# Optimization experiments

Hardware: AMD Instinct MI355X
Metric: run time of the kernel (lower is better)

Reference implementation:

```python
import jax, jax.numpy as jnp
import numpy as np

LAYER_BS = 63
N_SITES = 12
B = 2048


def _kaiming_uniform(key, shape, fan_in):
    # torch kaiming_uniform_ with a=0: bound = sqrt(6/fan_in)
    bound = np.sqrt(6.0 / fan_in)
    return jax.random.uniform(key, shape, jnp.float32, -bound, bound)


def _cnn12(x, w):
    # x: (B, L, 12, Cin); w: (L, 3*Cin, Cout)
    nn0 = jnp.roll(x, -1, axis=-2) + jnp.roll(x, 3, axis=-2)
    nnn0 = jnp.roll(x, -2, axis=-2) + jnp.roll(x, 4, axis=-2)
    c0 = jnp.concatenate([nn0, nnn0], axis=-1)          # (B,L,12,2*Cin)
    c1 = c0 + jnp.roll(c0, -2, axis=-2)
    allc = jnp.concatenate([x, c1], axis=-1)            # (B,L,12,3*Cin)
    return jnp.einsum('blsc,lco->blso', allc, w)


def _batch_linear(x, w, b):
    # x: (B, L, F); w: (L, F, O); b: (L, O)
    return jnp.einsum('blf,lfo->blo', x, w) + b


def setup_inputs() -> dict:
    key = jax.random.key(0)
    ks = jax.random.split(key, 9)
    zs = jax.random.normal(ks[0], (B, LAYER_BS, N_SITES, 2), jnp.float32)
    # CNN weights: (L, 3*Cin, Cout); kaiming fan_in = 3*Cin
    w1 = _kaiming_uniform(ks[1], (LAYER_BS, 6, 32), 6)
    w2 = _kaiming_uniform(ks[2], (LAYER_BS, 96, 64), 96)
    fw1 = _kaiming_uniform(ks[3], (LAYER_BS, 128, 64), 128)
    fb1 = jax.random.uniform(ks[4], (LAYER_BS, 64), jnp.float32, -1 / np.sqrt(128), 1 / np.sqrt(128))
    fw2 = _kaiming_uniform(ks[5], (LAYER_BS, 64, 64), 64)
    fb2 = jax.random.uniform(ks[6], (LAYER_BS, 64), jnp.float32, -1 / np.sqrt(64), 1 / np.sqrt(64))
    fw3 = _kaiming_uniform(ks[7], (LAYER_BS, 64, 1), 64)
    fb3 = jax.random.uniform(ks[8], (LAYER_BS, 1), jnp.float32, -1 / np.sqrt(64), 1 / np.sqrt(64))
    return {"zs": zs, "w1": w1, "w2": w2, "fw1": fw1, "fb1": fb1,
            "fw2": fw2, "fb2": fb2, "fw3": fw3, "fb3": fb3}


def reference(zs, w1, w2, fw1, fb1, fw2, fb2, fw3, fb3):
    h = jax.nn.relu(_cnn12(zs, w1))                     # (B,L,12,32)
    h = jax.nn.relu(_cnn12(h, w2))                      # (B,L,12,64)
    h = jnp.concatenate([h.mean(axis=-2), h.max(axis=-2)], axis=-1)
    h = jax.nn.relu(_batch_linear(h, fw1, fb1))
    h = jax.nn.relu(_batch_linear(h, fw2, fb2))
    out = _batch_linear(h, fw3, fb3)                    # (B,L,1)
    return out[..., 0]                                  # (B,L)
```

## Files before the change

### kernel.cpp

```cpp
#include <hip/hip_runtime.h>


#define LNUM 63
#define BT 16
#define NBT 128
#define WSL 19968

typedef __attribute__((ext_vector_type(8))) _Float16 half8;
typedef __attribute__((ext_vector_type(2))) _Float16 half2v;
typedef __attribute__((ext_vector_type(4))) float floatx4;
typedef __attribute__((ext_vector_type(4))) unsigned uint4v;

static __device__ __forceinline__ unsigned cvtpk(float a, float b) {
    return __builtin_bit_cast(unsigned, __builtin_amdgcn_cvt_pkrtz(a, b));
}
static __device__ __forceinline__ half2v u2h(unsigned u) { return __builtin_bit_cast(half2v, u); }
static __device__ __forceinline__ unsigned h2u(half2v h) { return __builtin_bit_cast(unsigned, h); }
static __device__ __forceinline__ float hlo16(unsigned short s) {
    return (float)__builtin_bit_cast(_Float16, s);
}
static __device__ __forceinline__ int w12(int v) { return v >= 12 ? v - 12 : v; }
static __device__ __forceinline__ float2 add2(float2 a, float2 b) { return make_float2(a.x + b.x, a.y + b.y); }

#define O_POOLDW 3072
#define O_POOLUS 6144
#define O_POOL2  0
#define O_G2     1280

__global__ void prep(const float* __restrict__ w2, const float* __restrict__ fw1,
                     const float* __restrict__ fw2, unsigned short* __restrict__ ws) {
    const int l = blockIdx.x, t = threadIdx.x;
    const int o = t & 63, g = t >> 6;
    if (blockIdx.y == 0) {
        unsigned* w2t = (unsigned*)(ws + (size_t)l * WSL);
        const float* w2l = w2 + (size_t)l * 6144;
        #pragma unroll
        for (int i = 0; i < 12; ++i) {
            int cp = g + 4 * i, c = 2 * cp;
            w2t[o * 52 + cp] = cvtpk(w2l[c * 64 + o], w2l[(c + 1) * 64 + o]);
        }
    } else {
        unsigned* f1t = (unsigned*)(ws + (size_t)l * WSL + 6656);
        const float* f1l = fw1 + (size_t)l * 8192;
        #pragma unroll
        for (int i = 0; i < 16; ++i) {
            int cp = g + 4 * i;
            f1t[o * 68 + cp] = cvtpk(f1l[cp * 64 + o], f1l[(64 + cp) * 64 + o]);
        }
        unsigned* f2t = (unsigned*)(ws + (size_t)l * WSL + 15360);
        const float* f2l = fw2 + (size_t)l * 4096;
        #pragma unroll
        for (int i = 0; i < 8; ++i) {
            int cp = g + 4 * i, c = 2 * cp;
            f2t[o * 36 + cp] = cvtpk(f2l[c * 64 + o], f2l[(c + 1) * 64 + o]);
        }
    }
}

__global__ __launch_bounds__(256, 4) void fused_nn(
    const float* __restrict__ zs,  const float* __restrict__ w1,
    const float* __restrict__ fb1, const float* __restrict__ fb2,
    const float* __restrict__ fw3, const float* __restrict__ fb3,
    const unsigned short* __restrict__ ws,
    float* __restrict__ out)
{
    __shared__ __align__(16) unsigned U[4160];
    unsigned short* USH = (unsigned short*)U;

    const int t    = threadIdx.x;
    const int lane = t & 63;
    const int wv   = t >> 6;
    const int n    = lane & 15;
    const int quad = lane >> 4;
    const int l    = blockIdx.x / NBT;
    const int b0   = (blockIdx.x % NBT) * BT;

    {
        const int b = t >> 4, cpair = t & 15, c0 = cpair * 2;
        const float* xb = zs + ((size_t)(b0 + b) * LNUM + l) * 24;
        float4 xq[6];
        #pragma unroll
        for (int q = 0; q < 6; ++q) xq[q] = *(const float4*)(xb + q * 4);
        float2 xv[12], xr[12], xA[12], xB[12];
        #pragma unroll
        for (int s = 0; s < 12; ++s)
            xv[s] = (s & 1) ? make_float2(xq[s >> 1].z, xq[s >> 1].w)
                            : make_float2(xq[s >> 1].x, xq[s >> 1].y);
        #pragma unroll
        for (int s = 0; s < 12; ++s) xr[s] = add2(xv[w12(s + 1)], xv[w12(s + 11)]);
        #pragma unroll
        for (int s = 0; s < 12; ++s) {
            xA[s] = add2(xr[w12(s + 2)], xr[w12(s + 10)]);
            xB[s] = add2(xr[w12(s + 3)], xr[w12(s + 9)]);
        }
        const float* wl = w1 + (size_t)l * 192 + c0;
        const float2 w0  = *(const float2*)(wl);
        const float2 w1v = *(const float2*)(wl + 32);
        const float2 w2v = *(const float2*)(wl + 64);
        const float2 w3v = *(const float2*)(wl + 96);
        const float2 w4v = *(const float2*)(wl + 128);
        const float2 w5v = *(const float2*)(wl + 160);
        #pragma unroll
        for (int s = 0; s < 12; ++s) {
            float hx = xv[s].x*w0.x + xv[s].y*w1v.x + xA[s].x*w2v.x + xA[s].y*w3v.x
                     + xB[s].x*w4v.x + xB[s].y*w5v.x;
            float hy = xv[s].x*w0.y + xv[s].y*w1v.y + xA[s].x*w2v.y + xA[s].y*w3v.y
                     + xB[s].x*w4v.y + xB[s].y*w5v.y;
            U[(b * 12 + s) * 20 + cpair] = cvtpk(fmaxf(hx, 0.f), fmaxf(hy, 0.f));
        }
    }
    const float bias1 = fb1[(size_t)l * 64 + wv * 16 + n];
    const float bias2 = fb2[(size_t)l * 64 + wv * 16 + n];
    __syncthreads();

    floatx4 acc[3][4];
    #pragma unroll
    for (int mi = 0; mi < 3; ++mi)
        #pragma unroll
        for (int nt = 0; nt < 4; ++nt) acc[mi][nt] = (floatx4){0.f, 0.f, 0.f, 0.f};
    {
        int bi[3], si[3];
        #pragma unroll
        for (int mi = 0; mi < 3; ++mi) {
            int row = 48 * wv + 16 * mi + n;
            bi[mi] = row / 12;
            si[mi] = row - 12 * bi[mi];
        }
        const int q4 = quad * 4;
        const uint4v* w2q = (const uint4v*)(ws + (size_t)l * WSL);
        const int dA[4] = {1, 11, 3, 9};
        const int dB[4] = {2, 10, 4, 8};
        #pragma unroll
        for (int ks = 0; ks < 3; ++ks) {
            uint4v bw[4];
            #pragma unroll
            for (int nt = 0; nt < 4; ++nt)
                bw[nt] = w2q[(nt * 16 + n) * 13 + ks * 4 + quad];
            half8 af[3];
            #pragma unroll
            for (int mi = 0; mi < 3; ++mi) {
                const int rb = bi[mi] * 12, s = si[mi];
                if (ks == 0) {
                    af[mi] = *(const half8*)(U + (rb + s) * 20 + q4);
                } else {
                    const int* d = (ks == 1) ? dA : dB;
                    half8 l0 = *(const half8*)(U + (rb + w12(s + d[0])) * 20 + q4);
                    half8 l1 = *(const half8*)(U + (rb + w12(s + d[1])) * 20 + q4);
                    half8 l2 = *(const half8*)(U + (rb + w12(s + d[2])) * 20 + q4);
                    half8 l3 = *(const half8*)(U + (rb + w12(s + d[3])) * 20 + q4);
                    af[mi] = (l0 + l1) + (l2 + l3);
                }
            }
            #pragma unroll
            for (int mi = 0; mi < 3; ++mi)
                #pragma unroll
                for (int nt = 0; nt < 4; ++nt)
                    acc[mi][nt] = __builtin_amdgcn_mfma_f32_16x16x32_f16(
                        af[mi], __builtin_bit_cast(half8, bw[nt]), acc[mi][nt], 0, 0, 0);
        }
    }
    __syncthreads();

    #pragma unroll
    for (int mi = 0; mi < 3; ++mi) {
        const int rr = 48 * wv + 16 * mi + 4 * quad;
        const int bq = rr / 12;
        const int chk = (rr - 12 * bq) >> 2;
        #pragma unroll
        for (int nt = 0; nt < 4; ++nt) {
            const int ch = nt * 16 + n;
            float r0 = fmaxf(acc[mi][nt][0], 0.f), r1 = fmaxf(acc[mi][nt][1], 0.f);
            float r2 = fmaxf(acc[mi][nt][2], 0.f), r3 = fmaxf(acc[mi][nt][3], 0.f);
            float sm = (r0 + r1) + (r2 + r3);
            float mx = fmaxf(fmaxf(r0, r1), fmaxf(r2, r3));
            U[(bq * 64 + ch) * 3 + chk] = cvtpk(sm, mx);
        }
    }
    __syncthreads();

    {
        const unsigned* p = U + t * 12;
        uint4v q0 = *(const uint4v*)(p);
        uint4v q1 = *(const uint4v*)(p + 4);
        uint4v q2 = *(const uint4v*)(p + 8);
        unsigned arr[12] = {q0.x, q0.y, q0.z, q0.w, q1.x, q1.y, q1.z, q1.w,
                            q2.x, q2.y, q2.z, q2.w};
        const int b = t >> 4, ch0 = (t * 4) & 63;
        const _Float16 inv12 = (_Float16)(1.0f / 12.0f);
        unsigned pk[4];
        #pragma unroll
        for (int j = 0; j < 4; ++j) {
            half2v d0 = u2h(arr[3 * j]), d1 = u2h(arr[3 * j + 1]), d2 = u2h(arr[3 * j + 2]);
            _Float16 s = (d0[0] + d1[0]) + d2[0];
            _Float16 m0 = d0[1] > d1[1] ? d0[1] : d1[1];
            _Float16 m  = m0 > d2[1] ? m0 : d2[1];
            half2v pm;
            pm[0] = s * inv12;
            pm[1] = m;
            pk[j] = h2u(pm);
        }
        uint2 w01 = make_uint2(pk[0], pk[1]), w23 = make_uint2(pk[2], pk[3]);
        *(uint2*)(U + O_POOLDW + b * 68 + ch0)     = w01;
        *(uint2*)(U + O_POOLDW + b * 68 + ch0 + 2) = w23;
    }
    __syncthreads();

    {
        const int o = wv * 16 + n;
        floatx4 a1 = (floatx4){bias1, bias1, bias1, bias1};
        const uint4v* f1q = (const uint4v*)(ws + (size_t)l * WSL + 6656);
        #pragma unroll
        for (int ks = 0; ks < 4; ++ks) {
            half8 av = *(const half8*)(USH + O_POOLUS + n * 136 + ks * 32 + quad * 8);
            uint4v bw = f1q[o * 17 + ks * 4 + quad];
            a1 = __builtin_amdgcn_mfma_f32_16x16x32_f16(av, __builtin_bit_cast(half8, bw), a1, 0, 0, 0);
        }
        #pragma unroll
        for (int i = 0; i < 2; ++i) {
            unsigned pk = cvtpk(fmaxf(a1[2 * i], 0.f), fmaxf(a1[2 * i + 1], 0.f));
            USH[O_POOL2 + (quad * 4 + 2 * i)     * 72 + o] = (unsigned short)(pk & 0xffffu);
            USH[O_POOL2 + (quad * 4 + 2 * i + 1) * 72 + o] = (unsigned short)(pk >> 16);
        }
    }
    __syncthreads();

    {
        const int o = wv * 16 + n;
        floatx4 a2 = (floatx4){bias2, bias2, bias2, bias2};
        const uint4v* f2q = (const uint4v*)(ws + (size_t)l * WSL + 15360);
        #pragma unroll
        for (int ks = 0; ks < 2; ++ks) {
            half8 av = *(const half8*)(USH + O_POOL2 + n * 72 + ks * 32 + quad * 8);
            uint4v bw = f2q[o * 9 + ks * 4 + quad];
            a2 = __builtin_amdgcn_mfma_f32_16x16x32_f16(av, __builtin_bit_cast(half8, bw), a2, 0, 0, 0);
        }
        #pragma unroll
        for (int i = 0; i < 2; ++i) {
            unsigned pk = cvtpk(fmaxf(a2[2 * i], 0.f), fmaxf(a2[2 * i + 1], 0.f));
            USH[O_G2 + (quad * 4 + 2 * i)     * 72 + o] = (unsigned short)(pk & 0xffffu);
            USH[O_G2 + (quad * 4 + 2 * i + 1) * 72 + o] = (unsigned short)(pk >> 16);
        }
    }
    __syncthreads();

    if (t < 16) {
        float a = fb3[l];
        const float* w3 = fw3 + (size_t)l * 64;
        #pragma unroll
        for (int c4 = 0; c4 < 16; ++c4) {
            uint2 u2 = *(const uint2*)(USH + O_G2 + t * 72 + c4 * 4);
            float4 w = *(const float4*)(w3 + c4 * 4);
            a += hlo16((unsigned short)(u2.x & 0xffff)) * w.x
               + hlo16((unsigned short)(u2.x >> 16))    * w.y
               + hlo16((unsigned short)(u2.y & 0xffff)) * w.z
               + hlo16((unsigned short)(u2.y >> 16))    * w.w;
        }
        out[(size_t)(b0 + t) * LNUM + l] = a;
    }
}

extern "C" void kernel_launch(void* const* d_in, const int* in_sizes, int n_in,
                              void* d_out, int out_size, void* d_ws, size_t ws_size,
                              hipStream_t stream) {
    const float* zs  = (const float*)d_in[0];
    const float* w1  = (const float*)d_in[1];
    const float* w2  = (const float*)d_in[2];
    const float* fw1 = (const float*)d_in[3];
    const float* fb1 = (const float*)d_in[4];
    const float* fw2 = (const float*)d_in[5];
    const float* fb2 = (const float*)d_in[6];
    const float* fw3 = (const float*)d_in[7];
    const float* fb3 = (const float*)d_in[8];
    float* out = (float*)d_out;
    unsigned short* ws = (unsigned short*)d_ws;

    hipLaunchKernelGGL(prep, dim3(LNUM, 2), dim3(256), 0, stream, w2, fw1, fw2, ws);
    hipLaunchKernelGGL(fused_nn, dim3(LNUM * NBT), dim3(256), 0, stream,
                       zs, w1, fb1, fb2, fw3, fb3, ws, out);
}
```

Baseline: 136.7 us.

## Halve batch tile to 8, pad site ring in LDS, widen per-wave FC outputs

Shrinks the per-block batch tile from 16 to 8 with 128 threads and twice as many blocks, and stores the first CNN layer output in a padded 20-row circular layout per batch so the neighbour gathers use fixed offsets instead of modular index math. The FC stages now give each of the two waves two 16-column output tiles. The aim is more blocks in flight, less LDS per block and cheaper address arithmetic, at the cost of duplicated halo writes and more total weight fetches from global memory across blocks. The FC stage with only 8 valid batch rows still feeds 16-row MFMA tiles, so half of each tile is wasted and the pooled-feature layout must stay consistent with the new offsets.

```diff
diff --git a/kernel.cpp b/kernel.cpp
--- a/kernel.cpp
+++ b/kernel.cpp
@@ -2,8 +2,9 @@
 
 
 #define LNUM 63
-#define BT 16
-#define NBT 128
+#define BT 8
+#define NBT 256
+#define TPB 128
 #define WSL 19968
 
 typedef __attribute__((ext_vector_type(8))) _Float16 half8;
@@ -15,15 +16,14 @@
     return __builtin_bit_cast(unsigned, __builtin_amdgcn_cvt_pkrtz(a, b));
 }
 static __device__ __forceinline__ half2v u2h(unsigned u) { return __builtin_bit_cast(half2v, u); }
-static __device__ __forceinline__ unsigned h2u(half2v h) { return __builtin_bit_cast(unsigned, h); }
 static __device__ __forceinline__ float hlo16(unsigned short s) {
     return (float)__builtin_bit_cast(_Float16, s);
 }
 static __device__ __forceinline__ int w12(int v) { return v >= 12 ? v - 12 : v; }
 static __device__ __forceinline__ float2 add2(float2 a, float2 b) { return make_float2(a.x + b.x, a.y + b.y); }
 
-#define O_POOLDW 3072
-#define O_POOLUS 6144
+#define O_POOLDW 1600
+#define O_POOLUS 3200
 #define O_POOL2  0
 #define O_G2     1280
 
@@ -57,14 +57,14 @@
     }
 }
 
-__global__ __launch_bounds__(256, 4) void fused_nn(
+__global__ __launch_bounds__(TPB, 4) void fused_nn(
     const float* __restrict__ zs,  const float* __restrict__ w1,
     const float* __restrict__ fb1, const float* __restrict__ fb2,
     const float* __restrict__ fw3, const float* __restrict__ fb3,
     const unsigned short* __restrict__ ws,
     float* __restrict__ out)
 {
-    __shared__ __align__(16) unsigned U[4160];
+    __shared__ __align__(16) unsigned U[3200];
     unsigned short* USH = (unsigned short*)U;
 
     const int t    = threadIdx.x;
@@ -100,17 +100,24 @@
         const float2 w3v = *(const float2*)(wl + 96);
         const float2 w4v = *(const float2*)(wl + 128);
         const float2 w5v = *(const float2*)(wl + 160);
+        unsigned* hb = U + (b * 20) * 20 + cpair;
         #pragma unroll
         for (int s = 0; s < 12; ++s) {
             float hx = xv[s].x*w0.x + xv[s].y*w1v.x + xA[s].x*w2v.x + xA[s].y*w3v.x
                      + xB[s].x*w4v.x + xB[s].y*w5v.x;
             float hy = xv[s].x*w0.y + xv[s].y*w1v.y + xA[s].x*w2v.y + xA[s].y*w3v.y
                      + xB[s].x*w4v.y + xB[s].y*w5v.y;
-            U[(b * 12 + s) * 20 + cpair] = cvtpk(fmaxf(hx, 0.f), fmaxf(hy, 0.f));
-        }
-    }
-    const float bias1 = fb1[(size_t)l * 64 + wv * 16 + n];
-    const float bias2 = fb2[(size_t)l * 64 + wv * 16 + n];
+            unsigned pk = cvtpk(fmaxf(hx, 0.f), fmaxf(hy, 0.f));
+            hb[(4 + s) * 20] = pk;
+            if (s <= 3) hb[(16 + s) * 20] = pk;
+            if (s >= 8) hb[(s - 8) * 20] = pk;
+        }
+    }
+    const int o0 = (2 * wv) * 16 + n;
+    const float bias1a = fb1[(size_t)l * 64 + o0];
+    const float bias1b = fb1[(size_t)l * 64 + o0 + 16];
+    const float bias2a = fb2[(size_t)l * 64 + o0];
+    const float bias2b = fb2[(size_t)l * 64 + o0 + 16];
     __syncthreads();
 
     floatx4 acc[3][4];
@@ -119,17 +126,14 @@
         #pragma unroll
         for (int nt = 0; nt < 4; ++nt) acc[mi][nt] = (floatx4){0.f, 0.f, 0.f, 0.f};
     {
-        int bi[3], si[3];
+        const unsigned* hbase[3];
         #pragma unroll
         for (int mi = 0; mi < 3; ++mi) {
             int row = 48 * wv + 16 * mi + n;
-            bi[mi] = row / 12;
-            si[mi] = row - 12 * bi[mi];
-        }
-        const int q4 = quad * 4;
+            int bi = row / 12, si = row - 12 * bi;
+            hbase[mi] = U + (bi * 20 + si) * 20 + quad * 4;
+        }
         const uint4v* w2q = (const uint4v*)(ws + (size_t)l * WSL);
-        const int dA[4] = {1, 11, 3, 9};
-        const int dB[4] = {2, 10, 4, 8};
         #pragma unroll
         for (int ks = 0; ks < 3; ++ks) {
             uint4v bw[4];
@@ -139,15 +143,20 @@
             half8 af[3];
             #pragma unroll
             for (int mi = 0; mi < 3; ++mi) {
-                const int rb = bi[mi] * 12, s = si[mi];
+                const unsigned* hb = hbase[mi];
                 if (ks == 0) {
-                    af[mi] = *(const half8*)(U + (rb + s) * 20 + q4);
+                    af[mi] = *(const half8*)(hb + 4 * 20);
+                } else if (ks == 1) {
+                    half8 l0 = *(const half8*)(hb + 5 * 20);
+                    half8 l1 = *(const half8*)(hb + 3 * 20);
+                    half8 l2 = *(const half8*)(hb + 7 * 20);
+                    half8 l3 = *(const half8*)(hb + 1 * 20);
+                    af[mi] = (l0 + l1) + (l2 + l3);
                 } else {
-                    const int* d = (ks == 1) ? dA : dB;
-                    half8 l0 = *(const half8*)(U + (rb + w12(s + d[0])) * 20 + q4);
-                    half8 l1 = *(const half8*)(U + (rb + w12(s + d[1])) * 20 + q4);
-                    half8 l2 = *(const half8*)(U + (rb + w12(s + d[2])) * 20 + q4);
-                    half8 l3 = *(const half8*)(U + (rb + w12(s + d[3])) * 20 + q4);
+                    half8 l0 = *(const half8*)(hb + 6 * 20);
+                    half8 l1 = *(const half8*)(hb + 2 * 20);
+                    half8 l2 = *(const half8*)(hb + 8 * 20);
+                    half8 l3 = *(const half8*)(hb + 0 * 20);
                     af[mi] = (l0 + l1) + (l2 + l3);
                 }
             }
@@ -197,7 +206,7 @@
             half2v pm;
             pm[0] = s * inv12;
             pm[1] = m;
-            pk[j] = h2u(pm);
+            pk[j] = __builtin_bit_cast(unsigned, pm);
         }
         uint2 w01 = make_uint2(pk[0], pk[1]), w23 = make_uint2(pk[2], pk[3]);
         *(uint2*)(U + O_POOLDW + b * 68 + ch0)     = w01;
@@ -206,44 +215,61 @@
     __syncthreads();
 
     {
-        const int o = wv * 16 + n;
-        floatx4 a1 = (floatx4){bias1, bias1, bias1, bias1};
+        floatx4 a1[2] = {(floatx4){bias1a, bias1a, bias1a, bias1a},
+                         (floatx4){bias1b, bias1b, bias1b, bias1b}};
         const uint4v* f1q = (const uint4v*)(ws + (size_t)l * WSL + 6656);
         #pragma unroll
         for (int ks = 0; ks < 4; ++ks) {
             half8 av = *(const half8*)(USH + O_POOLUS + n * 136 + ks * 32 + quad * 8);
-            uint4v bw = f1q[o * 17 + ks * 4 + quad];
-            a1 = __builtin_amdgcn_mfma_f32_16x16x32_f16(av, __builtin_bit_cast(half8, bw), a1, 0, 0, 0);
-        }
-        #pragma unroll
-        for (int i = 0; i < 2; ++i) {
-            unsigned pk = cvtpk(fmaxf(a1[2 * i], 0.f), fmaxf(a1[2 * i + 1], 0.f));
-            USH[O_POOL2 + (quad * 4 + 2 * i)     * 72 + o] = (unsigned short)(pk & 0xffffu);
-            USH[O_POOL2 + (quad * 4 + 2 * i + 1) * 72 + o] = (unsigned short)(pk >> 16);
-        }
-    }
-    __syncthreads();
-
-    {
-        const int o = wv * 16 + n;
-        floatx4 a2 = (floatx4){bias2, bias2, bias2, bias2};
+            #pragma unroll
+            for (int j = 0; j < 2; ++j) {
+                const int o = o0 + 16 * j;
+                uint4v bw = f1q[o * 17 + ks * 4 + quad];
+                a1[j] = __builtin_amdgcn_mfma_f32_16x16x32_f16(av, __builtin_bit_cast(half8, bw), a1[j], 0, 0, 0);
+            }
+        }
+        __syncthreads();
+        #pragma unroll
+        for (int j = 0; j < 2; ++j) {
+            const int o = o0 + 16 * j;
+            #pragma unroll
+            for (int i = 0; i < 2; ++i) {
+                unsigned pk = cvtpk(fmaxf(a1[j][2 * i], 0.f), fmaxf(a1[j][2 * i + 1], 0.f));
+                USH[O_POOL2 + (quad * 4 + 2 * i)     * 72 + o] = (unsigned short)(pk & 0xffffu);
+                USH[O_POOL2 + (quad * 4 + 2 * i + 1) * 72 + o] = (unsigned short)(pk >> 16);
+            }
+        }
+    }
+    __syncthreads();
+
+    {
+        floatx4 a2[2] = {(floatx4){bias2a, bias2a, bias2a, bias2a},
+                         (floatx4){bias2b, bias2b, bias2b, bias2b}};
         const uint4v* f2q = (const uint4v*)(ws + (size_t)l * WSL + 15360);
         #pragma unroll
         for (int ks = 0; ks < 2; ++ks) {
             half8 av = *(const half8*)(USH + O_POOL2 + n * 72 + ks * 32 + quad * 8);
-            uint4v bw = f2q[o * 9 + ks * 4 + quad];
-            a2 = __builtin_amdgcn_mfma_f32_16x16x32_f16(av, __builtin_bit_cast(half8, bw), a2, 0, 0, 0);
-        }
-        #pragma unroll
-        for (int i = 0; i < 2; ++i) {
-            unsigned pk = cvtpk(fmaxf(a2[2 * i], 0.f), fmaxf(a2[2 * i + 1], 0.f));
-            USH[O_G2 + (quad * 4 + 2 * i)     * 72 + o] = (unsigned short)(pk & 0xffffu);
-            USH[O_G2 + (quad * 4 + 2 * i + 1) * 72 + o] = (unsigned short)(pk >> 16);
-        }
-    }
-    __syncthreads();
-
-    if (t < 16) {
+            #pragma unroll
+            for (int j = 0; j < 2; ++j) {
+                const int o = o0 + 16 * j;
+                uint4v bw = f2q[o * 9 + ks * 4 + quad];
+                a2[j] = __builtin_amdgcn_mfma_f32_16x16x32_f16(av, __builtin_bit_cast(half8, bw), a2[j], 0, 0, 0);
+            }
+        }
+        #pragma unroll
+        for (int j = 0; j < 2; ++j) {
+            const int o = o0 + 16 * j;
+            #pragma unroll
+            for (int i = 0; i < 2; ++i) {
+                unsigned pk = cvtpk(fmaxf(a2[j][2 * i], 0.f), fmaxf(a2[j][2 * i + 1], 0.f));
+                USH[O_G2 + (quad * 4 + 2 * i)     * 72 + o] = (unsigned short)(pk & 0xffffu);
+                USH[O_G2 + (quad * 4 + 2 * i + 1) * 72 + o] = (unsigned short)(pk >> 16);
+            }
+        }
+    }
+    __syncthreads();
+
+    if (t < BT) {
         float a = fb3[l];
         const float* w3 = fw3 + (size_t)l * 64;
         #pragma unroll
@@ -275,6 +301,6 @@
     unsigned short* ws = (unsigned short*)d_ws;
 
     hipLaunchKernelGGL(prep, dim3(LNUM, 2), dim3(256), 0, stream, w2, fw1, fw2, ws);
-    hipLaunchKernelGGL(fused_nn, dim3(LNUM * NBT), dim3(256), 0, stream,
+    hipLaunchKernelGGL(fused_nn, dim3(LNUM * NBT), dim3(TPB), 0, stream,
                        zs, w1, fb1, fb2, fw3, fb3, ws, out);
 }
```

Measured after the change: 147.5 us. 1.08x slower.
